# Kernel tuning notes

Measured on AMD Instinct MI355X. Metric: run time of the kernel, lower is better.

Reference implementation:

```python
import jax, jax.numpy as jnp
import numpy as np

HIDDEN = 1024
N_HEAD = 16
HEAD_DIM = HIDDEN // N_HEAD

def setup_inputs() -> dict:
    key = jax.random.key(0)
    ks = jax.random.split(key, 5)
    B, T = 2, 2048
    s_in = 1.0 / np.sqrt(HIDDEN)
    return {
        "x": jax.random.normal(ks[0], (B, T, HIDDEN), dtype=jnp.float32),
        "w_attn": jax.random.normal(ks[1], (HIDDEN, 3 * HIDDEN), dtype=jnp.float32) * s_in,
        "b_attn": jnp.zeros((3 * HIDDEN,), dtype=jnp.float32),
        "w_proj": jax.random.normal(ks[2], (HIDDEN, HIDDEN), dtype=jnp.float32) * s_in,
        "b_proj": jnp.zeros((HIDDEN,), dtype=jnp.float32),
    }

def reference(x, w_attn, b_attn, w_proj, b_proj):
    B, T, C = x.shape
    qkv = x @ w_attn + b_attn  # (B, T, 3C)
    q, k, v = jnp.split(qkv, 3, axis=-1)
    # (B, H, T, D)
    q = q.reshape(B, T, N_HEAD, HEAD_DIM).transpose(0, 2, 1, 3)
    k = k.reshape(B, T, N_HEAD, HEAD_DIM).transpose(0, 2, 1, 3)
    v = v.reshape(B, T, N_HEAD, HEAD_DIM).transpose(0, 2, 1, 3)
    scale = 1.0 / np.sqrt(HEAD_DIM).astype(np.float32)
    attn = jnp.einsum('bhqd,bhkd->bhqk', q, k) * scale
    causal = jnp.tril(jnp.ones((T, T), dtype=bool))
    attn = jnp.where(causal[None, None], attn, -jnp.inf)
    attn = jax.nn.softmax(attn, axis=-1)
    out = jnp.einsum('bhqk,bhkd->bhqd', attn, v)
    out = out.transpose(0, 2, 1, 3).reshape(B, T, C)
    return out @ w_proj + b_proj
```

## Files before the change

### kernel.cpp

```cpp
#include <hip/hip_runtime.h>
#include <stdint.h>

#define T_SEQ 2048
#define NB 2
#define NH 16
#define HD 64
#define HID 1024
#define MTOK (NB * T_SEQ)

typedef float f32x4 __attribute__((ext_vector_type(4)));
typedef float f32x16 __attribute__((ext_vector_type(16)));
typedef short bf16x8 __attribute__((ext_vector_type(8)));
typedef unsigned short u16;
typedef unsigned int u32;

#define QSCALE 0.1803368801f

__device__ __forceinline__ u16 f2bf(float f) {
  union { float f; uint32_t u; } v; v.f = f;
  return (u16)((v.u + 0x7fffu + ((v.u >> 16) & 1u)) >> 16);
}

__device__ __forceinline__ void gl_lds16(const void* g, void* l) {
  __builtin_amdgcn_global_load_lds(
      (const __attribute__((address_space(1))) unsigned int*)g,
      (__attribute__((address_space(3))) unsigned int*)l, 16, 0, 0);
}

__global__ void convert_k(const float* __restrict__ in, u16* __restrict__ out, int n4) {
  int i = blockIdx.x * blockDim.x + threadIdx.x;
  int stride = gridDim.x * blockDim.x;
  for (; i < n4; i += stride) {
    float4 f = ((const float4*)in)[i];
    ushort4 o;
    o.x = f2bf(f.x); o.y = f2bf(f.y); o.z = f2bf(f.z); o.w = f2bf(f.w);
    ((ushort4*)out)[i] = o;
  }
}

__global__ void transpose_k(const float* __restrict__ in, u16* __restrict__ out, int R, int C) {
  __shared__ float tile[32][33];
  int c0 = blockIdx.x * 32, r0 = blockIdx.y * 32;
  int tx = threadIdx.x, ty = threadIdx.y;
#pragma unroll
  for (int i = 0; i < 32; i += 8)
    tile[ty + i][tx] = in[(size_t)(r0 + ty + i) * C + c0 + tx];
  __syncthreads();
#pragma unroll
  for (int i = 0; i < 32; i += 8)
    out[(size_t)(c0 + ty + i) * R + r0 + tx] = f2bf(tile[tx][ty + i]);
}

template <int MODE>
__global__ __launch_bounds__(512, 6)
void gemm_k(const u16* __restrict__ A, const u16* __restrict__ Bt,
            const float* __restrict__ bias,
            u16* __restrict__ q, u16* __restrict__ kk, u16* __restrict__ v,
            float* __restrict__ outf) {
  __shared__ __align__(16) char lds[49152];
  const int tid = threadIdx.x, wid = tid >> 6, lane = tid & 63;
  const int m0 = blockIdx.y * 128, n0 = blockIdx.x * 128;
  const int wm = (wid >> 2) * 64, wn = (wid & 3) * 32;

  f32x4 acc[4][2];
  const f32x4 z = {0.f, 0.f, 0.f, 0.f};
#pragma unroll
  for (int mi = 0; mi < 4; ++mi)
#pragma unroll
    for (int ni = 0; ni < 2; ++ni) acc[mi][ni] = z;

  const int srow = tid >> 2;
  const int scb = (tid & 3) << 4;
  const int scsrc = (scb ^ ((srow & 3) << 4)) >> 1;
  const int rA = lane & 15;
  const int kbyte = (lane >> 4) << 4;

#define GSTAGE(tt_, bi_)                                                      \
  do {                                                                        \
    const int k0_ = (tt_) << 5;                                               \
    char* ab_ = lds + (bi_) * 16384;                                          \
    char* bb_ = ab_ + 8192;                                                   \
    gl_lds16(A + (size_t)(m0 + srow) * HID + k0_ + scsrc, ab_ + wid * 1024);  \
    gl_lds16(Bt + (size_t)(n0 + srow) * HID + k0_ + scsrc, bb_ + wid * 1024); \
  } while (0)

  GSTAGE(0, 0);
  GSTAGE(1, 1);
  GSTAGE(2, 2);

  int cur = 0;
  for (int tt = 0; tt < 32; ++tt) {
    if (tt < 30)       asm volatile("s_waitcnt vmcnt(4)" ::: "memory");
    else if (tt == 30) asm volatile("s_waitcnt vmcnt(2)" ::: "memory");
    else               asm volatile("s_waitcnt vmcnt(0)" ::: "memory");
    __builtin_amdgcn_s_barrier();
    __builtin_amdgcn_sched_barrier(0);

    const char* ab = lds + cur * 16384;
    const char* bb = ab + 8192;
    bf16x8 a[4], b[2];
#pragma unroll
    for (int mi = 0; mi < 4; ++mi) {
      const int row = wm + mi * 16 + rA;
      a[mi] = *(const bf16x8*)(ab + row * 64 + (kbyte ^ ((row & 3) << 4)));
    }
#pragma unroll
    for (int ni = 0; ni < 2; ++ni) {
      const int row = wn + ni * 16 + rA;
      b[ni] = *(const bf16x8*)(bb + row * 64 + (kbyte ^ ((row & 3) << 4)));
    }
#pragma unroll
    for (int mi = 0; mi < 4; ++mi)
#pragma unroll
      for (int ni = 0; ni < 2; ++ni)
        acc[mi][ni] = __builtin_amdgcn_mfma_f32_16x16x32_bf16(a[mi], b[ni], acc[mi][ni], 0, 0, 0);

    __builtin_amdgcn_s_barrier();
    __builtin_amdgcn_sched_barrier(0);
    if (tt + 3 < 32) GSTAGE(tt + 3, cur);
    cur = (cur == 2) ? 0 : cur + 1;
  }
#undef GSTAGE

  const int coll = lane & 15, rowl = (lane >> 4) << 2;
#pragma unroll
  for (int mi = 0; mi < 4; ++mi) {
#pragma unroll
    for (int ni = 0; ni < 2; ++ni) {
      const int n = n0 + wn + ni * 16 + coll;
      const float bv = bias[n];
#pragma unroll
      for (int r = 0; r < 4; ++r) {
        const int m = m0 + wm + mi * 16 + rowl + r;
        float val = acc[mi][ni][r] + bv;
        if (MODE == 0) {
          const int reg = n >> 10, c = n & 1023, h = c >> 6, d = c & 63;
          const int bb2 = m >> 11, t = m & 2047;
          if (reg == 0) q[((size_t)(bb2 * NH + h) * T_SEQ + t) * HD + d] = f2bf(val * QSCALE);
          else if (reg == 1) kk[((size_t)(bb2 * NH + h) * T_SEQ + t) * HD + d] = f2bf(val);
          else v[((size_t)(bb2 * NH + h) * HD + d) * T_SEQ + t] = f2bf(val);
        } else {
          outf[(size_t)m * HID + n] = val;
        }
      }
    }
  }
}

__global__ __launch_bounds__(512, 4)
void attn_k(const u16* __restrict__ Q, const u16* __restrict__ K,
            const u16* __restrict__ Vt, u16* __restrict__ AO) {
  __shared__ __align__(16) char lds[65536];
  const int tid = threadIdx.x;
  const int lane = tid & 63;
  const int wid = tid >> 6;
  const int qsub = wid & 3, par = wid >> 2;
  const int bid = blockIdx.x;
  const int halfg = bid >> 8, r8 = bid & 255;
  const int bh = (r8 & 7) * 4 + ((r8 >> 3) & 3);
  const int lvl = r8 >> 5;
  const int qb = halfg ? lvl : (15 - lvl);
  const int q0 = qb * 128;
  const int ql = lane & 31, h = lane >> 5;
  const bool hi = (h != 0);

  const u16* Qg = Q + (size_t)bh * T_SEQ * HD;
  const u16* Kg = K + (size_t)bh * T_SEQ * HD;
  const u16* Vg = Vt + (size_t)bh * T_SEQ * HD;

  const int q0w = q0 + qsub * 32;
  const int dq = 2 * qb + (qsub >> 1);

  bf16x8 qf[4];
#pragma unroll
  for (int s = 0; s < 4; ++s)
    qf[s] = *(const bf16x8*)(Qg + (size_t)(q0w + ql) * HD + s * 16 + h * 8);

  f32x16 ot0, ot1;
#pragma unroll
  for (int i = 0; i < 16; ++i) { ot0[i] = 0.f; ot1[i] = 0.f; }
  float m = -3.0e38f, l = 0.f;

  const int srow = tid >> 3;
  const int scb = (tid & 7) << 4;
  const int sc0 = (scb ^ ((srow & 7) << 4)) >> 1;

  const int nsup = qb + 1;

#define STAGE(tt_)                                                            \
  do {                                                                        \
    const int kv0_ = (tt_) << 6;                                              \
    gl_lds16(Kg + (size_t)(kv0_ + srow) * HD + sc0,                           \
             lds + (((tt_) & 3) << 13) + wid * 1024);                         \
    gl_lds16(Vg + (size_t)srow * T_SEQ + kv0_ + sc0,                          \
             lds + 32768 + (((tt_) & 3) << 13) + wid * 1024);                 \
  } while (0)

  STAGE(0);
  STAGE(1);

  for (int ss = 0; ss < nsup; ++ss) {
    if (ss + 1 < nsup) {
      STAGE(2 * ss + 2);
      STAGE(2 * ss + 3);
      asm volatile("s_waitcnt vmcnt(4)" ::: "memory");
    } else {
      asm volatile("s_waitcnt vmcnt(0)" ::: "memory");
    }
    __builtin_amdgcn_s_barrier();
    __builtin_amdgcn_sched_barrier(0);

    const int tt = 2 * ss + par;
    if (tt <= dq) {
      const int kv0 = tt << 6;
      const char* kb = lds + ((tt & 3) << 13);
      const char* vb = lds + 32768 + ((tt & 3) << 13);
      f32x16 s0, s1;
#pragma unroll
      for (int i = 0; i < 16; ++i) { s0[i] = 0.f; s1[i] = 0.f; }
#pragma unroll
      for (int s = 0; s < 4; ++s) {
        const int cb = 32 * s + 16 * h;
        const int r0 = ql, r1 = 32 + ql;
        bf16x8 kf0 = *(const bf16x8*)(kb + r0 * 128 + (cb ^ ((r0 & 7) << 4)));
        bf16x8 kf1 = *(const bf16x8*)(kb + r1 * 128 + (cb ^ ((r1 & 7) << 4)));
        s0 = __builtin_amdgcn_mfma_f32_32x32x16_bf16(kf0, qf[s], s0, 0, 0, 0);
        s1 = __builtin_amdgcn_mfma_f32_32x32x16_bf16(kf1, qf[s], s1, 0, 0, 0);
      }
      if (tt == dq) {
        const int qg = q0w + ql;
#pragma unroll
        for (int r = 0; r < 16; ++r) {
          const int kvl = (r & 3) + 8 * (r >> 2) + 4 * h;
          if (kv0 + kvl > qg) s0[r] = -3.0e38f;
          if (kv0 + 32 + kvl > qg) s1[r] = -3.0e38f;
        }
      }
      float mx[16];
#pragma unroll
      for (int i = 0; i < 16; ++i) mx[i] = fmaxf(s0[i], s1[i]);
#pragma unroll
      for (int d = 8; d; d >>= 1)
#pragma unroll
        for (int i = 0; i < d; ++i) mx[i] = fmaxf(mx[i], mx[i + d]);
      const float tm = fmaxf(mx[0], __shfl_xor(mx[0], 32, 64));
      if (!__all(tm <= m + 4.0f)) {
        const float mnew = fmaxf(m, tm);
        const float fold = __builtin_amdgcn_exp2f(m - mnew);
        m = mnew;
        l *= fold;
#pragma unroll
        for (int i = 0; i < 16; ++i) { ot0[i] *= fold; ot1[i] *= fold; }
      }
#pragma unroll
      for (int i = 0; i < 16; ++i) {
        s0[i] = __builtin_amdgcn_exp2f(s0[i] - m);
        s1[i] = __builtin_amdgcn_exp2f(s1[i] - m);
      }
      float sm[16];
#pragma unroll
      for (int i = 0; i < 16; ++i) sm[i] = s0[i] + s1[i];
#pragma unroll
      for (int d = 8; d; d >>= 1)
#pragma unroll
        for (int i = 0; i < d; ++i) sm[i] += sm[i + d];
      l += sm[0] + __shfl_xor(sm[0], 32, 64);

      u32 w0[8], w1[8];
#pragma unroll
      for (int mm = 0; mm < 8; ++mm) {
        asm("v_cvt_pk_bf16_f32 %0, %1, %2" : "=v"(w0[mm]) : "v"(s0[2 * mm]), "v"(s0[2 * mm + 1]));
        asm("v_cvt_pk_bf16_f32 %0, %1, %2" : "=v"(w1[mm]) : "v"(s1[2 * mm]), "v"(s1[2 * mm + 1]));
      }
#pragma unroll
      for (int sb = 0; sb < 2; ++sb) {
#pragma unroll
        for (int t = 0; t < 2; ++t) {
          u32 a0 = sb ? w1[4 * t]     : w0[4 * t];
          u32 a1 = sb ? w1[4 * t + 1] : w0[4 * t + 1];
          u32 a2 = sb ? w1[4 * t + 2] : w0[4 * t + 2];
          u32 a3 = sb ? w1[4 * t + 3] : w0[4 * t + 3];
          u32 snd0 = hi ? a0 : a2;
          u32 snd1 = hi ? a1 : a3;
          u32 own0 = hi ? a2 : a0;
          u32 own1 = hi ? a3 : a1;
          u32 p0 = __shfl_xor(snd0, 32, 64);
          u32 p1 = __shfl_xor(snd1, 32, 64);
          union { u32 u[4]; bf16x8 v; } fr;
          fr.u[0] = hi ? p0 : own0;
          fr.u[1] = hi ? p1 : own1;
          fr.u[2] = hi ? own0 : p0;
          fr.u[3] = hi ? own1 : p1;
          const int s = sb * 2 + t;
          const int cb = 32 * s + 16 * h;
          const int r0 = ql, r1 = 32 + ql;
          bf16x8 vf0 = *(const bf16x8*)(vb + r0 * 128 + (cb ^ ((r0 & 7) << 4)));
          bf16x8 vf1 = *(const bf16x8*)(vb + r1 * 128 + (cb ^ ((r1 & 7) << 4)));
          ot0 = __builtin_amdgcn_mfma_f32_32x32x16_bf16(vf0, fr.v, ot0, 0, 0, 0);
          ot1 = __builtin_amdgcn_mfma_f32_32x32x16_bf16(vf1, fr.v, ot1, 0, 0, 0);
        }
      }
    }
    __builtin_amdgcn_s_barrier();
    __builtin_amdgcn_sched_barrier(0);
  }
#undef STAGE

  float* R = (float*)(lds + qsub * 8448);
  if (par == 1) {
#pragma unroll
    for (int r = 0; r < 16; ++r) {
      const int dl = (r & 3) + 8 * (r >> 2) + 4 * h;
      R[ql * 66 + dl] = ot0[r];
      R[ql * 66 + 32 + dl] = ot1[r];
    }
    if (!hi) { R[ql * 66 + 64] = m; R[ql * 66 + 65] = l; }
  }
  __builtin_amdgcn_s_barrier();
  if (par == 1) return;

  const float m2 = R[ql * 66 + 64];
  const float l2 = R[ql * 66 + 65];
  const float M = fmaxf(m, m2);
  const float c1 = __builtin_amdgcn_exp2f(m - M);
  const float c2 = __builtin_amdgcn_exp2f(m2 - M);
  const float L = c1 * l + c2 * l2;
  const float inv = 1.0f / L;
  float of0[16], of1[16];
#pragma unroll
  for (int r = 0; r < 16; ++r) {
    const int dl = (r & 3) + 8 * (r >> 2) + 4 * h;
    of0[r] = (c1 * ot0[r] + c2 * R[ql * 66 + dl]) * inv;
    of1[r] = (c1 * ot1[r] + c2 * R[ql * 66 + 32 + dl]) * inv;
  }
  asm volatile("s_waitcnt lgkmcnt(0)" ::: "memory");
  __builtin_amdgcn_sched_barrier(0);

  float* E = (float*)(lds + qsub * 8448);
#pragma unroll
  for (int r = 0; r < 16; ++r) {
    const int dl = (r & 3) + 8 * (r >> 2) + 4 * h;
    E[dl * 33 + ql] = of0[r];
    E[(dl + 32) * 33 + ql] = of1[r];
  }
  asm volatile("s_waitcnt lgkmcnt(0)" ::: "memory");
  __builtin_amdgcn_sched_barrier(0);
  const int bb = bh >> 4, hh = bh & 15;
  const int r2 = lane >> 3;
  const int c8 = (lane & 7) * 8;
#pragma unroll
  for (int g = 0; g < 4; ++g) {
    const int qrow = g * 8 + r2;
    union { u16 a[8]; bf16x8 v; } ov;
#pragma unroll
    for (int j = 0; j < 8; ++j) ov.a[j] = f2bf(E[(c8 + j) * 33 + qrow]);
    *(bf16x8*)(AO + (size_t)(bb * T_SEQ + q0 + qsub * 32 + qrow) * HID + hh * HD + c8) = ov.v;
  }
}

extern "C" void kernel_launch(void* const* d_in, const int* in_sizes, int n_in,
                              void* d_out, int out_size, void* d_ws, size_t ws_size,
                              hipStream_t stream) {
  const float* x      = (const float*)d_in[0];
  const float* w_attn = (const float*)d_in[1];
  const float* b_attn = (const float*)d_in[2];
  const float* w_proj = (const float*)d_in[3];
  const float* b_proj = (const float*)d_in[4];
  float* out = (float*)d_out;

  char* ws = (char*)d_ws;
  u16* xb   = (u16*)(ws);
  u16* wabT = (u16*)(ws + (size_t)(8  << 20));
  u16* wpbT = (u16*)(ws + (size_t)(14 << 20));
  u16* q    = (u16*)(ws + (size_t)(16 << 20));
  u16* k    = (u16*)(ws + (size_t)(24 << 20));
  u16* v    = (u16*)(ws + (size_t)(32 << 20));
  u16* ao   = (u16*)(ws + (size_t)(40 << 20));

  convert_k<<<dim3(1024), dim3(256), 0, stream>>>(x, xb, MTOK * HID / 4);
  transpose_k<<<dim3(96, 32), dim3(32, 8), 0, stream>>>(w_attn, wabT, HID, 3 * HID);
  transpose_k<<<dim3(32, 32), dim3(32, 8), 0, stream>>>(w_proj, wpbT, HID, HID);
  gemm_k<0><<<dim3(24, 32), dim3(512), 0, stream>>>(xb, wabT, b_attn, q, k, v, nullptr);
  attn_k<<<dim3(512), dim3(512), 0, stream>>>(q, k, v, ao);
  gemm_k<1><<<dim3(8, 32), dim3(512), 0, stream>>>(ao, wpbT, b_proj, nullptr, nullptr, nullptr, out);
}
```

Baseline: 107.5 us.

## Fuse prep kernels, vectorize V epilogue stores, raise MFMA wave priority

Merges the x conversion and both weight transposes into one launch, so two kernel launches and their gaps go away. The QKV GEMM epilogue now branches once per block on region and writes the transposed V output as packed 4-element bf16 stores instead of scalar ones. It also adds s_setprio around the MFMA sections in the attention kernel, so waves issuing matrix ops get scheduling priority. The risks are extra branch divergence in the combined prep kernel and priority effects that are hard to predict.

```diff
diff --git a/kernel.cpp b/kernel.cpp
--- a/kernel.cpp
+++ b/kernel.cpp
@@ -27,21 +27,36 @@
       (__attribute__((address_space(3))) unsigned int*)l, 16, 0, 0);
 }
 
-__global__ void convert_k(const float* __restrict__ in, u16* __restrict__ out, int n4) {
-  int i = blockIdx.x * blockDim.x + threadIdx.x;
-  int stride = gridDim.x * blockDim.x;
-  for (; i < n4; i += stride) {
-    float4 f = ((const float4*)in)[i];
-    ushort4 o;
-    o.x = f2bf(f.x); o.y = f2bf(f.y); o.z = f2bf(f.z); o.w = f2bf(f.w);
-    ((ushort4*)out)[i] = o;
-  }
-}
-
-__global__ void transpose_k(const float* __restrict__ in, u16* __restrict__ out, int R, int C) {
+__global__ __launch_bounds__(256)
+void prep_k(const float* __restrict__ x, u16* __restrict__ xb,
+            const float* __restrict__ wa, u16* __restrict__ waT,
+            const float* __restrict__ wp, u16* __restrict__ wpT) {
   __shared__ float tile[32][33];
-  int c0 = blockIdx.x * 32, r0 = blockIdx.y * 32;
-  int tx = threadIdx.x, ty = threadIdx.y;
+  const int bid = blockIdx.x, tid = threadIdx.x;
+  if (bid < 1024) {
+    int i = bid * 1024 + tid;
+#pragma unroll
+    for (int it = 0; it < 4; ++it, i += 256) {
+      float4 f = ((const float4*)x)[i];
+      ushort4 o;
+      o.x = f2bf(f.x); o.y = f2bf(f.y); o.z = f2bf(f.z); o.w = f2bf(f.w);
+      ((ushort4*)xb)[i] = o;
+    }
+    return;
+  }
+  const float* in;
+  u16* out;
+  int R, C, c0, r0;
+  if (bid < 4096) {
+    const int j = bid - 1024;
+    in = wa; out = waT; R = HID; C = 3 * HID;
+    c0 = (j % 96) * 32; r0 = (j / 96) * 32;
+  } else {
+    const int j = bid - 4096;
+    in = wp; out = wpT; R = HID; C = HID;
+    c0 = (j % 32) * 32; r0 = (j / 32) * 32;
+  }
+  const int tx = tid & 31, ty = tid >> 5;
 #pragma unroll
   for (int i = 0; i < 32; i += 8)
     tile[ty + i][tx] = in[(size_t)(r0 + ty + i) * C + c0 + tx];
@@ -123,24 +138,56 @@
 #undef GSTAGE
 
   const int coll = lane & 15, rowl = (lane >> 4) << 2;
-#pragma unroll
-  for (int mi = 0; mi < 4; ++mi) {
-#pragma unroll
-    for (int ni = 0; ni < 2; ++ni) {
-      const int n = n0 + wn + ni * 16 + coll;
-      const float bv = bias[n];
-#pragma unroll
-      for (int r = 0; r < 4; ++r) {
-        const int m = m0 + wm + mi * 16 + rowl + r;
-        float val = acc[mi][ni][r] + bv;
-        if (MODE == 0) {
-          const int reg = n >> 10, c = n & 1023, h = c >> 6, d = c & 63;
-          const int bb2 = m >> 11, t = m & 2047;
-          if (reg == 0) q[((size_t)(bb2 * NH + h) * T_SEQ + t) * HD + d] = f2bf(val * QSCALE);
-          else if (reg == 1) kk[((size_t)(bb2 * NH + h) * T_SEQ + t) * HD + d] = f2bf(val);
-          else v[((size_t)(bb2 * NH + h) * HD + d) * T_SEQ + t] = f2bf(val);
-        } else {
-          outf[(size_t)m * HID + n] = val;
+  if (MODE == 0) {
+    const int reg = n0 >> 10;
+    const int bb2 = m0 >> 11;
+    const int tloc = (m0 & 2047) + wm;
+    if (reg == 2) {
+#pragma unroll
+      for (int mi = 0; mi < 4; ++mi) {
+#pragma unroll
+        for (int ni = 0; ni < 2; ++ni) {
+          const int n = n0 + wn + ni * 16 + coll;
+          const float bv = bias[n];
+          const int c = n & 1023, h = c >> 6, d = c & 63;
+          ushort4 pk;
+          pk.x = f2bf(acc[mi][ni][0] + bv);
+          pk.y = f2bf(acc[mi][ni][1] + bv);
+          pk.z = f2bf(acc[mi][ni][2] + bv);
+          pk.w = f2bf(acc[mi][ni][3] + bv);
+          const int t0 = tloc + mi * 16 + rowl;
+          *(ushort4*)(v + ((size_t)(bb2 * NH + h) * HD + d) * T_SEQ + t0) = pk;
+        }
+      }
+    } else {
+      u16* dst = (reg == 0) ? q : kk;
+      const float sc = (reg == 0) ? QSCALE : 1.0f;
+#pragma unroll
+      for (int mi = 0; mi < 4; ++mi) {
+#pragma unroll
+        for (int ni = 0; ni < 2; ++ni) {
+          const int n = n0 + wn + ni * 16 + coll;
+          const float bv = bias[n];
+          const int c = n & 1023, h = c >> 6, d = c & 63;
+#pragma unroll
+          for (int r = 0; r < 4; ++r) {
+            const int t = tloc + mi * 16 + rowl + r;
+            dst[((size_t)(bb2 * NH + h) * T_SEQ + t) * HD + d] = f2bf((acc[mi][ni][r] + bv) * sc);
+          }
+        }
+      }
+    }
+  } else {
+#pragma unroll
+    for (int mi = 0; mi < 4; ++mi) {
+#pragma unroll
+      for (int ni = 0; ni < 2; ++ni) {
+        const int n = n0 + wn + ni * 16 + coll;
+        const float bv = bias[n];
+#pragma unroll
+        for (int r = 0; r < 4; ++r) {
+          const int m = m0 + wm + mi * 16 + rowl + r;
+          outf[(size_t)m * HID + n] = acc[mi][ni][r] + bv;
         }
       }
     }
@@ -218,6 +265,7 @@
       f32x16 s0, s1;
 #pragma unroll
       for (int i = 0; i < 16; ++i) { s0[i] = 0.f; s1[i] = 0.f; }
+      __builtin_amdgcn_s_setprio(1);
 #pragma unroll
       for (int s = 0; s < 4; ++s) {
         const int cb = 32 * s + 16 * h;
@@ -227,6 +275,7 @@
         s0 = __builtin_amdgcn_mfma_f32_32x32x16_bf16(kf0, qf[s], s0, 0, 0, 0);
         s1 = __builtin_amdgcn_mfma_f32_32x32x16_bf16(kf1, qf[s], s1, 0, 0, 0);
       }
+      __builtin_amdgcn_s_setprio(0);
       if (tt == dq) {
         const int qg = q0w + ql;
 #pragma unroll
@@ -272,6 +321,7 @@
         asm("v_cvt_pk_bf16_f32 %0, %1, %2" : "=v"(w0[mm]) : "v"(s0[2 * mm]), "v"(s0[2 * mm + 1]));
         asm("v_cvt_pk_bf16_f32 %0, %1, %2" : "=v"(w1[mm]) : "v"(s1[2 * mm]), "v"(s1[2 * mm + 1]));
       }
+      __builtin_amdgcn_s_setprio(1);
 #pragma unroll
       for (int sb = 0; sb < 2; ++sb) {
 #pragma unroll
@@ -300,6 +350,7 @@
           ot1 = __builtin_amdgcn_mfma_f32_32x32x16_bf16(vf1, fr.v, ot1, 0, 0, 0);
         }
       }
+      __builtin_amdgcn_s_setprio(0);
     }
     __builtin_amdgcn_s_barrier();
     __builtin_amdgcn_sched_barrier(0);
@@ -377,9 +428,7 @@
   u16* v    = (u16*)(ws + (size_t)(32 << 20));
   u16* ao   = (u16*)(ws + (size_t)(40 << 20));
 
-  convert_k<<<dim3(1024), dim3(256), 0, stream>>>(x, xb, MTOK * HID / 4);
-  transpose_k<<<dim3(96, 32), dim3(32, 8), 0, stream>>>(w_attn, wabT, HID, 3 * HID);
-  transpose_k<<<dim3(32, 32), dim3(32, 8), 0, stream>>>(w_proj, wpbT, HID, HID);
+  prep_k<<<dim3(5120), dim3(256), 0, stream>>>(x, xb, w_attn, wabT, w_proj, wpbT);
   gemm_k<0><<<dim3(24, 32), dim3(512), 0, stream>>>(xb, wabT, b_attn, q, k, v, nullptr);
   attn_k<<<dim3(512), dim3(512), 0, stream>>>(q, k, v, ao);
   gemm_k<1><<<dim3(8, 32), dim3(512), 0, stream>>>(ao, wpbT, b_proj, nullptr, nullptr, nullptr, out);
```

After: 98.62 us. 1.09x faster.
